# Performance work log

Measured on AMD Instinct MI355X. Metric: run time of the kernel, lower is better.

Reference implementation:

```python
import jax, jax.numpy as jnp
import numpy as np
import math

L = 3        # n_layers
H = 8        # n_heads
D = 128      # embed_dim
KD = D // H  # key_dim = val_dim = 16
FF = 512     # feed_forward_hidden
B, N = 200, 100
BN = B * N
E = 320000
EPS = 1e-5   # BatchNorm1d eps


def setup_inputs() -> dict:
    key = jax.random.key(0)
    ks = jax.random.split(key, 12)

    def u(k, shape, last):  # torch uniform(-1/sqrt(last), 1/sqrt(last)) init
        s = 1.0 / math.sqrt(last)
        return jax.random.uniform(k, shape, jnp.float32, -s, s)

    x = jax.random.normal(ks[0], (B, N, D), jnp.float32)
    edge_index = jax.random.randint(ks[1], (2, E), 0, BN, jnp.int32)
    return {
        "x": x,
        "edge_index": edge_index,
        "Wq": u(ks[2], (L, H, D, KD), KD),
        "Wk": u(ks[3], (L, H, D, KD), KD),
        "Wv": u(ks[4], (L, H, D, KD), KD),
        "Wout": u(ks[5], (L, H, KD, D), D),
        "bn1_w": jnp.ones((L, D), jnp.float32),
        "bn1_b": jnp.zeros((L, D), jnp.float32),
        "W1": u(ks[6], (L, D, FF), D),
        "b1": u(ks[7], (L, FF), D),
        "W2": u(ks[8], (L, FF, D), FF),
        "b2": u(ks[9], (L, D), FF),
        "bn2_w": jnp.ones((L, D), jnp.float32),
        "bn2_b": jnp.zeros((L, D), jnp.float32),
    }


def _batch_norm(h, w, b):
    # BatchNorm1d over flattened (B*N, D), training-mode batch stats (biased var)
    flat = h.reshape(-1, h.shape[-1])
    mu = flat.mean(axis=0)
    var = flat.var(axis=0)
    y = (flat - mu) / jnp.sqrt(var + EPS) * w + b
    return y.reshape(h.shape)


def _gat_conv(h, src, dst, Wq, Wk, Wv, Wout):
    Bb, Nn, Dd = h.shape
    bn = Bb * Nn
    flat = h.reshape(bn, Dd)
    Hh, _, Kk = Wq.shape
    # faithful to torch: matmul gives [H, BN, K], then raw .view(BN, H, K)
    Q = jnp.einsum('nd,hdk->hnk', flat, Wq).reshape(bn, Hh, Kk)
    Kt = jnp.einsum('nd,hdk->hnk', flat, Wk).reshape(bn, Hh, Kk)
    V = jnp.einsum('nd,hdk->hnk', flat, Wv).reshape(bn, Hh, Kk)
    norm = 1.0 / math.sqrt(Kk)
    # message: Q_j (source) . K_i (target) per edge, per head -> [E, H]
    attn = norm * jnp.sum(Q[src] * Kt[dst], axis=-1)
    # segment softmax over edges grouped by target node (max detached, as in PyG)
    m = jax.lax.stop_gradient(jax.ops.segment_max(attn, dst, num_segments=bn))
    ex = jnp.exp(attn - m[dst])
    s = jax.ops.segment_sum(ex, dst, num_segments=bn)
    a = ex / (s[dst] + 1e-16)
    # weighted V_i scatter-added into target nodes -> [BN, H, K]
    aggr = jax.ops.segment_sum(V[dst] * a[:, :, None], dst, num_segments=bn)
    out = aggr.reshape(bn, Hh * Kk) @ Wout.reshape(Hh * Kk, -1)
    return out.reshape(Bb, Nn, -1)


def reference(x, edge_index, Wq, Wk, Wv, Wout, bn1_w, bn1_b, W1, b1, W2, b2, bn2_w, bn2_b):
    src, dst = edge_index[0], edge_index[1]
    h = x
    for l in range(L):
        h = h + _gat_conv(h, src, dst, Wq[l], Wk[l], Wv[l], Wout[l])
        h = _batch_norm(h, bn1_w[l], bn1_b[l])
        ff = jnp.maximum(h @ W1[l] + b1[l], 0.0) @ W2[l] + b2[l]
        h = h + ff
        h = _batch_norm(h, bn2_w[l], bn2_b[l])
    return h
```

## Files before the change

### kernel.cpp

```cpp
#include <hip/hip_runtime.h>
#include <hip/hip_bf16.h>

#define BN_ 20000
#define D_ 128
#define FF_ 512
#define E_ 320000
#define NBLK 313
#define LSTR 136
#define TSTR 72
#define B2STR 72

typedef __attribute__((ext_vector_type(8))) short bf16x8;
typedef __attribute__((ext_vector_type(4))) float f32x4;

__device__ __forceinline__ unsigned short f2b(float f) {
    unsigned int u = __float_as_uint(f);
    u = (u + 0x7FFFu + ((u >> 16) & 1u)) >> 16;
    return (unsigned short)u;
}

__device__ __forceinline__ void make_ss(const float* __restrict__ acc,
                                        const float* __restrict__ w,
                                        const float* __restrict__ b,
                                        float* __restrict__ ss_sh, int tid) {
    if (tid < 128) {
        if (acc) {
            float s = acc[tid], q = acc[128 + tid];
            float mu  = s * (1.f / 20000.f);
            float var = fmaxf(q * (1.f / 20000.f) - mu * mu, 0.f);
            float rstd  = rsqrtf(var + 1e-5f);
            float scale = w[tid] * rstd;
            ss_sh[tid]       = scale;
            ss_sh[128 + tid] = b[tid] - mu * scale;
        } else {
            ss_sh[tid]       = 1.f;
            ss_sh[128 + tid] = 0.f;
        }
    }
}

__global__ __launch_bounds__(256) void k_prep(const float* __restrict__ Wv,
                                              const float* __restrict__ Wout,
                                              const float* __restrict__ W1,
                                              const float* __restrict__ W2,
                                              unsigned short* __restrict__ WcT,
                                              unsigned short* __restrict__ WoT,
                                              unsigned short* __restrict__ W1T,
                                              unsigned short* __restrict__ W2T,
                                              float* __restrict__ flag,
                                              float* __restrict__ acc6) {
    int idx = blockIdx.x * 256 + threadIdx.x;
    if (idx < 49152) {
        int l = idx / 16384, r = idx % 16384;
        int n = r >> 7, k = r & 127;
        int h = n >> 4, kk = n & 15;
        WcT[idx] = f2b(Wv[((l * 8 + h) * 128 + k) * 16 + kk]);
        return;
    }
    idx -= 49152;
    if (idx < 49152) {
        int l = idx / 16384, r = idx % 16384;
        int n = r >> 7, k = r & 127;
        WoT[idx] = f2b(Wout[l * 16384 + k * 128 + n]);
        return;
    }
    idx -= 49152;
    if (idx < 196608) {
        int l = idx / 65536, r = idx % 65536;
        int n = r >> 7, k = r & 127;
        W1T[idx] = f2b(W1[l * 65536 + k * 512 + n]);
        return;
    }
    idx -= 196608;
    if (idx < 196608) {
        int l = idx / 65536, r = idx % 65536;
        int n = r / 512, k = r % 512;
        W2T[idx] = f2b(W2[l * 65536 + k * 128 + n]);
        return;
    }
    idx -= 196608;
    if (idx < 20000) { flag[idx] = 0.f; return; }
    idx -= 20000;
    if (idx < 1536) acc6[idx] = 0.f;
}

__global__ __launch_bounds__(256) void k_flag(const int* __restrict__ dst,
                                              float* __restrict__ flag) {
    int e = blockIdx.x * 256 + threadIdx.x;
    if (e < E_) flag[dst[e]] = 1.0f;
}


__global__ __launch_bounds__(256) void k_vs(const float* __restrict__ H,
                                            const float* __restrict__ accP,
                                            const float* __restrict__ bnw,
                                            const float* __restrict__ bnb,
                                            const unsigned short* __restrict__ Bt,
                                            unsigned short* __restrict__ Vs) {
    __shared__ unsigned short As[64 * LSTR];
    __shared__ unsigned short Bs[64 * LSTR];
    __shared__ float ss_sh[256];
    const int tid = threadIdx.x;
    const int row0 = blockIdx.x * 64, col0 = blockIdx.y * 64;
    make_ss(accP, bnw, bnb, ss_sh, tid);
    __syncthreads();
#pragma unroll
    for (int it = 0; it < 4; ++it) {
        int idx = tid + it * 256;
        int m = idx >> 4, k0 = (idx & 15) << 3;
        int gr = row0 + m;
        float v[8];
        if (gr < BN_) {
            f32x4 v0 = *(const f32x4*)(H + gr * D_ + k0);
            f32x4 v1 = *(const f32x4*)(H + gr * D_ + k0 + 4);
            v[0] = v0.x; v[1] = v0.y; v[2] = v0.z; v[3] = v0.w;
            v[4] = v1.x; v[5] = v1.y; v[6] = v1.z; v[7] = v1.w;
        } else {
#pragma unroll
            for (int j = 0; j < 8; ++j) v[j] = 0.f;
        }
        unsigned int p[4];
#pragma unroll
        for (int j = 0; j < 4; ++j) {
            unsigned short lo = f2b(v[2 * j] * ss_sh[k0 + 2 * j] + ss_sh[128 + k0 + 2 * j]);
            unsigned short hi = f2b(v[2 * j + 1] * ss_sh[k0 + 2 * j + 1] + ss_sh[128 + k0 + 2 * j + 1]);
            p[j] = (unsigned int)lo | ((unsigned int)hi << 16);
        }
        *(uint4*)&As[m * LSTR + k0] = make_uint4(p[0], p[1], p[2], p[3]);
    }
#pragma unroll
    for (int it = 0; it < 4; ++it) {
        int idx = tid + it * 256;
        int n = idx >> 4, k0 = (idx & 15) << 3;
        *(uint4*)&Bs[n * LSTR + k0] = *(const uint4*)(Bt + (col0 + n) * D_ + k0);
    }
    __syncthreads();
    const int lane = tid & 63, wave = tid >> 6;
    const int l16 = lane & 15, quad = lane >> 4;
    const int wm = (wave >> 1) * 32, wn = (wave & 1) * 32;
    f32x4 acc[2][2] = {};
#pragma unroll
    for (int kb = 0; kb < 128; kb += 32) {
        bf16x8 a0 = *(bf16x8*)&As[(wm + l16) * LSTR + kb + quad * 8];
        bf16x8 a1 = *(bf16x8*)&As[(wm + 16 + l16) * LSTR + kb + quad * 8];
        bf16x8 b0 = *(bf16x8*)&Bs[(wn + l16) * LSTR + kb + quad * 8];
        bf16x8 b1 = *(bf16x8*)&Bs[(wn + 16 + l16) * LSTR + kb + quad * 8];
        acc[0][0] = __builtin_amdgcn_mfma_f32_16x16x32_bf16(a0, b0, acc[0][0], 0, 0, 0);
        acc[0][1] = __builtin_amdgcn_mfma_f32_16x16x32_bf16(a0, b1, acc[0][1], 0, 0, 0);
        acc[1][0] = __builtin_amdgcn_mfma_f32_16x16x32_bf16(a1, b0, acc[1][0], 0, 0, 0);
        acc[1][1] = __builtin_amdgcn_mfma_f32_16x16x32_bf16(a1, b1, acc[1][1], 0, 0, 0);
    }
#pragma unroll
    for (int i = 0; i < 2; ++i)
#pragma unroll
        for (int j = 0; j < 2; ++j) {
            int gc = col0 + wn + j * 16 + l16;
            int h = gc >> 4, kk = gc & 15;
#pragma unroll
            for (int r = 0; r < 4; ++r) {
                int gr = row0 + wm + i * 16 + quad * 4 + r;
                if (gr < BN_) Vs[h * (BN_ * 16) + gr * 16 + kk] = f2b(acc[i][j][r]);
            }
        }
}

__global__ __launch_bounds__(256) void k_out(const unsigned short* __restrict__ Vs,
                                             const unsigned short* __restrict__ Bt,
                                             const float* __restrict__ H,
                                             const float* __restrict__ accP,
                                             const float* __restrict__ bnw,
                                             const float* __restrict__ bnb,
                                             const float* __restrict__ flag,
                                             float* __restrict__ H1,
                                             float* __restrict__ accO) {
    __shared__ unsigned short As[64 * LSTR];
    __shared__ unsigned short Bs[64 * LSTR];
    __shared__ float ss_sh[256];
    const int tid = threadIdx.x;
    const int row0 = blockIdx.x * 64, col0 = blockIdx.y * 64;
    make_ss(accP, bnw, bnb, ss_sh, tid);
#pragma unroll
    for (int it = 0; it < 4; ++it) {
        int idx = tid + it * 256;
        int m = idx >> 4, k0 = (idx & 15) << 3;
        int gr = row0 + m;
        uint4 w = make_uint4(0u, 0u, 0u, 0u);
        if (gr < BN_) w = *(const uint4*)(Vs + gr * D_ + k0);
        *(uint4*)&As[m * LSTR + k0] = w;
    }
#pragma unroll
    for (int it = 0; it < 4; ++it) {
        int idx = tid + it * 256;
        int n = idx >> 4, k0 = (idx & 15) << 3;
        *(uint4*)&Bs[n * LSTR + k0] = *(const uint4*)(Bt + (col0 + n) * D_ + k0);
    }
    __syncthreads();
    const int lane = tid & 63, wave = tid >> 6;
    const int l16 = lane & 15, quad = lane >> 4;
    const int wm = (wave >> 1) * 32, wn = (wave & 1) * 32;
    f32x4 acc[2][2] = {};
#pragma unroll
    for (int kb = 0; kb < 128; kb += 32) {
        bf16x8 a0 = *(bf16x8*)&As[(wm + l16) * LSTR + kb + quad * 8];
        bf16x8 a1 = *(bf16x8*)&As[(wm + 16 + l16) * LSTR + kb + quad * 8];
        bf16x8 b0 = *(bf16x8*)&Bs[(wn + l16) * LSTR + kb + quad * 8];
        bf16x8 b1 = *(bf16x8*)&Bs[(wn + 16 + l16) * LSTR + kb + quad * 8];
        acc[0][0] = __builtin_amdgcn_mfma_f32_16x16x32_bf16(a0, b0, acc[0][0], 0, 0, 0);
        acc[0][1] = __builtin_amdgcn_mfma_f32_16x16x32_bf16(a0, b1, acc[0][1], 0, 0, 0);
        acc[1][0] = __builtin_amdgcn_mfma_f32_16x16x32_bf16(a1, b0, acc[1][0], 0, 0, 0);
        acc[1][1] = __builtin_amdgcn_mfma_f32_16x16x32_bf16(a1, b1, acc[1][1], 0, 0, 0);
    }
    __syncthreads();
    float* Sred = (float*)As;
    float* Qred = (float*)Bs;
    const int slot = (wave >> 1) * 4 + quad;
#pragma unroll
    for (int j = 0; j < 2; ++j) {
        int gc = col0 + wn + j * 16 + l16;
        float sc = ss_sh[gc & 127];
        float sh = ss_sh[128 + (gc & 127)];
        float cs = 0.f, cq = 0.f;
#pragma unroll
        for (int i = 0; i < 2; ++i)
#pragma unroll
            for (int r = 0; r < 4; ++r) {
                int gr = row0 + wm + i * 16 + quad * 4 + r;
                if (gr < BN_) {
                    float z = H[gr * D_ + gc] * sc + sh;
                    float o = z + flag[gr] * acc[i][j][r];
                    H1[gr * D_ + gc] = o;
                    cs += o; cq += o * o;
                }
            }
        Sred[(wn + j * 16 + l16) * 8 + slot] = cs;
        Qred[(wn + j * 16 + l16) * 8 + slot] = cq;
    }
    __syncthreads();
    if (tid < 64) {
        float s = 0.f, q = 0.f;
#pragma unroll
        for (int t = 0; t < 8; ++t) { s += Sred[tid * 8 + t]; q += Qred[tid * 8 + t]; }
        atomicAdd(&accO[col0 + tid], s);
        atomicAdd(&accO[128 + col0 + tid], q);
    }
}

__global__ __launch_bounds__(256) void k_ff(const float* __restrict__ H1,
                                            const float* __restrict__ accP,
                                            const float* __restrict__ bnw,
                                            const float* __restrict__ bnb,
                                            const unsigned short* __restrict__ W1t,
                                            const float* __restrict__ b1l,
                                            const unsigned short* __restrict__ W2t,
                                            const float* __restrict__ b2l,
                                            float* __restrict__ H2,
                                            float* __restrict__ accO) {
    __shared__ unsigned short As[64 * LSTR];
    __shared__ unsigned short Bs[64 * LSTR];
    __shared__ unsigned short B2[128 * B2STR];
    __shared__ unsigned short Tch[64 * TSTR];
    __shared__ float ss_sh[256];
    const int tid = threadIdx.x;
    const int row0 = blockIdx.x * 64;
    make_ss(accP, bnw, bnb, ss_sh, tid);
    __syncthreads();
#pragma unroll
    for (int it = 0; it < 4; ++it) {
        int idx = tid + it * 256;
        int m = idx >> 4, k0 = (idx & 15) << 3;
        int gr = row0 + m;
        float v[8];
        if (gr < BN_) {
            f32x4 v0 = *(const f32x4*)(H1 + gr * D_ + k0);
            f32x4 v1 = *(const f32x4*)(H1 + gr * D_ + k0 + 4);
            v[0] = v0.x; v[1] = v0.y; v[2] = v0.z; v[3] = v0.w;
            v[4] = v1.x; v[5] = v1.y; v[6] = v1.z; v[7] = v1.w;
        } else {
#pragma unroll
            for (int j = 0; j < 8; ++j) v[j] = 0.f;
        }
        unsigned int p[4];
#pragma unroll
        for (int j = 0; j < 4; ++j) {
            unsigned short lo = f2b(v[2 * j] * ss_sh[k0 + 2 * j] + ss_sh[128 + k0 + 2 * j]);
            unsigned short hi = f2b(v[2 * j + 1] * ss_sh[k0 + 2 * j + 1] + ss_sh[128 + k0 + 2 * j + 1]);
            p[j] = (unsigned int)lo | ((unsigned int)hi << 16);
        }
        *(uint4*)&As[m * LSTR + k0] = make_uint4(p[0], p[1], p[2], p[3]);
    }
    const int lane = tid & 63, wave = tid >> 6;
    const int l16 = lane & 15, quad = lane >> 4;
    const int wm = (wave >> 1) * 32;
    const int wn = (wave & 1) * 32;
    const int wn2 = (wave & 1) * 64;
    f32x4 acc2[2][4] = {};
    for (int c = 0; c < 8; ++c) {
        const int cb = c * 64;
        __syncthreads();
#pragma unroll
        for (int it = 0; it < 4; ++it) {
            int idx = tid + it * 256;
            int n = idx >> 4, k0 = (idx & 15) << 3;
            *(uint4*)&Bs[n * LSTR + k0] = *(const uint4*)(W1t + (cb + n) * D_ + k0);
        }
#pragma unroll
        for (int it = 0; it < 4; ++it) {
            int idx = tid + it * 256;
            int n = idx >> 3, k0 = (idx & 7) << 3;
            *(uint4*)&B2[n * B2STR + k0] = *(const uint4*)(W2t + n * FF_ + cb + k0);
        }
        __syncthreads();
        f32x4 acc1[2][2] = {};
#pragma unroll
        for (int kb = 0; kb < 128; kb += 32) {
            bf16x8 a0 = *(bf16x8*)&As[(wm + l16) * LSTR + kb + quad * 8];
            bf16x8 a1 = *(bf16x8*)&As[(wm + 16 + l16) * LSTR + kb + quad * 8];
            bf16x8 b0 = *(bf16x8*)&Bs[(wn + l16) * LSTR + kb + quad * 8];
            bf16x8 b1 = *(bf16x8*)&Bs[(wn + 16 + l16) * LSTR + kb + quad * 8];
            acc1[0][0] = __builtin_amdgcn_mfma_f32_16x16x32_bf16(a0, b0, acc1[0][0], 0, 0, 0);
            acc1[0][1] = __builtin_amdgcn_mfma_f32_16x16x32_bf16(a0, b1, acc1[0][1], 0, 0, 0);
            acc1[1][0] = __builtin_amdgcn_mfma_f32_16x16x32_bf16(a1, b0, acc1[1][0], 0, 0, 0);
            acc1[1][1] = __builtin_amdgcn_mfma_f32_16x16x32_bf16(a1, b1, acc1[1][1], 0, 0, 0);
        }
#pragma unroll
        for (int j = 0; j < 2; ++j) {
            int lc = wn + j * 16 + l16;
            float bb = b1l[cb + lc];
#pragma unroll
            for (int i = 0; i < 2; ++i)
#pragma unroll
                for (int r = 0; r < 4; ++r)
                    Tch[(wm + i * 16 + quad * 4 + r) * TSTR + lc] =
                        f2b(fmaxf(acc1[i][j][r] + bb, 0.f));
        }
        __syncthreads();
#pragma unroll
        for (int kb = 0; kb < 64; kb += 32) {
            bf16x8 a0 = *(bf16x8*)&Tch[(wm + l16) * TSTR + kb + quad * 8];
            bf16x8 a1 = *(bf16x8*)&Tch[(wm + 16 + l16) * TSTR + kb + quad * 8];
#pragma unroll
            for (int j2 = 0; j2 < 4; ++j2) {
                bf16x8 b = *(bf16x8*)&B2[(wn2 + j2 * 16 + l16) * B2STR + kb + quad * 8];
                acc2[0][j2] = __builtin_amdgcn_mfma_f32_16x16x32_bf16(a0, b, acc2[0][j2], 0, 0, 0);
                acc2[1][j2] = __builtin_amdgcn_mfma_f32_16x16x32_bf16(a1, b, acc2[1][j2], 0, 0, 0);
            }
        }
    }
    __syncthreads();
    float* Sred = (float*)As;
    float* Qred = (float*)Bs;
    const int slot = (wave >> 1) * 4 + quad;
#pragma unroll
    for (int j2 = 0; j2 < 4; ++j2) {
        int gc = wn2 + j2 * 16 + l16;
        float sc = ss_sh[gc], sh = ss_sh[128 + gc], bb = b2l[gc];
        float cs = 0.f, cq = 0.f;
#pragma unroll
        for (int i = 0; i < 2; ++i)
#pragma unroll
            for (int r = 0; r < 4; ++r) {
                int gr = row0 + wm + i * 16 + quad * 4 + r;
                if (gr < BN_) {
                    float o = H1[gr * D_ + gc] * sc + sh + acc2[i][j2][r] + bb;
                    H2[gr * D_ + gc] = o;
                    cs += o; cq += o * o;
                }
            }
        Sred[gc * 8 + slot] = cs;
        Qred[gc * 8 + slot] = cq;
    }
    __syncthreads();
    if (tid < 128) {
        float s = 0.f, q = 0.f;
#pragma unroll
        for (int t = 0; t < 8; ++t) { s += Sred[tid * 8 + t]; q += Qred[tid * 8 + t]; }
        atomicAdd(&accO[tid], s);
        atomicAdd(&accO[128 + tid], q);
    }
}

__global__ __launch_bounds__(256) void k_apply(const float4* __restrict__ H2,
                                               const float* __restrict__ accP,
                                               const float* __restrict__ bnw,
                                               const float* __restrict__ bnb,
                                               float4* __restrict__ out) {
    __shared__ float ss_sh[256];
    make_ss(accP, bnw, bnb, ss_sh, threadIdx.x);
    __syncthreads();
    int i = blockIdx.x * 256 + threadIdx.x;
    if (i >= BN_ * D_ / 4) return;
    int c = (i & 31) << 2;
    float4 v = H2[i];
    v.x = v.x * ss_sh[c + 0] + ss_sh[128 + c + 0];
    v.y = v.y * ss_sh[c + 1] + ss_sh[128 + c + 1];
    v.z = v.z * ss_sh[c + 2] + ss_sh[128 + c + 2];
    v.w = v.w * ss_sh[c + 3] + ss_sh[128 + c + 3];
    out[i] = v;
}


extern "C" void kernel_launch(void* const* d_in, const int* in_sizes, int n_in,
                              void* d_out, int out_size, void* d_ws, size_t ws_size,
                              hipStream_t stream) {
    (void)in_sizes; (void)n_in; (void)out_size; (void)ws_size;
    const float* x    = (const float*)d_in[0];
    const int*   edge = (const int*)d_in[1];
    const float* Wv   = (const float*)d_in[4];
    const float* Wout = (const float*)d_in[5];
    const float* bn1w = (const float*)d_in[6];
    const float* bn1b = (const float*)d_in[7];
    const float* W1   = (const float*)d_in[8];
    const float* b1   = (const float*)d_in[9];
    const float* W2   = (const float*)d_in[10];
    const float* b2   = (const float*)d_in[11];
    const float* bn2w = (const float*)d_in[12];
    const float* bn2b = (const float*)d_in[13];

    float* ws   = (float*)d_ws;
    float* bufA = ws;
    float* bufB = ws + 2560000;
    float* flag = ws + 5120000;
    float* acc6 = ws + 5140000;
    unsigned short* Vs  = (unsigned short*)(ws + 5141536);
    unsigned short* WcT = (unsigned short*)(ws + 6421536);
    unsigned short* WoT = (unsigned short*)(ws + 6446112);
    unsigned short* W1T = (unsigned short*)(ws + 6470688);
    unsigned short* W2T = (unsigned short*)(ws + 6568992);

    k_prep<<<2005, 256, 0, stream>>>(Wv, Wout, W1, W2, WcT, WoT, W1T, W2T,
                                     flag, acc6);
    k_flag<<<1250, 256, 0, stream>>>(edge + E_, flag);

    for (int l = 0; l < 3; ++l) {
        const float* Hc   = (l == 0) ? x : bufA;
        const float* accP = (l == 0) ? nullptr : acc6 + (2 * l - 1) * 256;
        float* acc1p = acc6 + (2 * l) * 256;
        float* acc2p = acc6 + (2 * l + 1) * 256;
        const float* bw  = bn2w + (l ? (l - 1) * 128 : 0);
        const float* bbv = bn2b + (l ? (l - 1) * 128 : 0);
        k_vs<<<dim3(NBLK, 2), 256, 0, stream>>>(Hc, accP, bw, bbv,
                                                WcT + l * 16384, Vs);
        k_out<<<dim3(NBLK, 2), 256, 0, stream>>>(Vs, WoT + l * 16384, Hc, accP,
                                                 bw, bbv, flag, bufB, acc1p);
        k_ff<<<NBLK, 256, 0, stream>>>(bufB, acc1p, bn1w + l * 128, bn1b + l * 128,
                                       W1T + l * 65536, b1 + l * 512,
                                       W2T + l * 65536, b2 + l * 128, bufA, acc2p);
    }
    k_apply<<<2500, 256, 0, stream>>>((const float4*)bufA, acc6 + 5 * 256,
                                      bn2w + 256, bn2b + 256, (float4*)d_out);
}
```

Measured before the change: 251.4 us.

## Fuse all layers into one persistent kernel with software grid barriers

Replaces the chain of per-layer launches (prep, flag, vs, out, ff, apply) with a single persistent kernel of 313 blocks that uses an atomic-counter grid barrier between dependent stages. Weight conversion, flag setting, the V/out/FF GEMMs and the final BN apply are all done inside it, with each block owning a 64-row tile. This removes launch gaps and inter-kernel drains. In exchange it relies on all 313 blocks being co-resident, otherwise the barrier deadlocks, and it adds barrier spin cost. The merged kernel's combined LDS footprint may also reduce occupancy.

Result: slower. 950.8 us (+278.2%).

```diff
diff --git a/kernel.cpp b/kernel.cpp
--- a/kernel.cpp
+++ b/kernel.cpp
@@ -5,7 +5,7 @@
 #define D_ 128
 #define FF_ 512
 #define E_ 320000
-#define NBLK 313
+#define NB_ 313
 #define LSTR 136
 #define TSTR 72
 #define B2STR 72
@@ -39,363 +39,373 @@
     }
 }
 
-__global__ __launch_bounds__(256) void k_prep(const float* __restrict__ Wv,
-                                              const float* __restrict__ Wout,
-                                              const float* __restrict__ W1,
-                                              const float* __restrict__ W2,
-                                              unsigned short* __restrict__ WcT,
-                                              unsigned short* __restrict__ WoT,
-                                              unsigned short* __restrict__ W1T,
-                                              unsigned short* __restrict__ W2T,
-                                              float* __restrict__ flag,
-                                              float* __restrict__ acc6) {
-    int idx = blockIdx.x * 256 + threadIdx.x;
-    if (idx < 49152) {
+__device__ __forceinline__ void gbar(int* __restrict__ bar) {
+    __builtin_amdgcn_fence(__ATOMIC_RELEASE, "agent");
+    __syncthreads();
+    if (threadIdx.x == 0) {
+        int* cnt = bar;
+        int* gen = bar + 1;
+        int g = __hip_atomic_load(gen, __ATOMIC_RELAXED, __HIP_MEMORY_SCOPE_AGENT);
+        int prev = __hip_atomic_fetch_add(cnt, 1, __ATOMIC_ACQ_REL, __HIP_MEMORY_SCOPE_AGENT);
+        if (prev == NB_ - 1) {
+            __hip_atomic_store(cnt, 0, __ATOMIC_RELAXED, __HIP_MEMORY_SCOPE_AGENT);
+            __hip_atomic_fetch_add(gen, 1, __ATOMIC_ACQ_REL, __HIP_MEMORY_SCOPE_AGENT);
+        } else {
+            while (__hip_atomic_load(gen, __ATOMIC_RELAXED, __HIP_MEMORY_SCOPE_AGENT) == g)
+                __builtin_amdgcn_s_sleep(2);
+        }
+    }
+    __syncthreads();
+    __builtin_amdgcn_fence(__ATOMIC_ACQUIRE, "agent");
+}
+
+__global__ __launch_bounds__(256) void k_init(float* __restrict__ flag,
+                                              float* __restrict__ acc6,
+                                              int* __restrict__ bar) {
+    int i = blockIdx.x * 256 + threadIdx.x;
+    if (i < BN_) flag[i] = 0.f;
+    if (i < 1536) acc6[i] = 0.f;
+    if (i < 2) bar[i] = 0;
+}
+
+__global__ __launch_bounds__(256, 2) void k_main(
+    const float* __restrict__ x, const int* __restrict__ dst,
+    const float* __restrict__ Wv, const float* __restrict__ Wout,
+    const float* __restrict__ bn1w, const float* __restrict__ bn1b,
+    const float* __restrict__ W1, const float* __restrict__ b1,
+    const float* __restrict__ W2, const float* __restrict__ b2,
+    const float* __restrict__ bn2w, const float* __restrict__ bn2b,
+    float* __restrict__ bufA, float* __restrict__ bufB,
+    float* __restrict__ flag, float* __restrict__ acc6,
+    unsigned short* __restrict__ Vs,
+    unsigned short* __restrict__ WcT, unsigned short* __restrict__ WoT,
+    unsigned short* __restrict__ W1T, unsigned short* __restrict__ W2T,
+    int* __restrict__ bar, float* __restrict__ out) {
+    __shared__ unsigned short As[64 * LSTR];
+    __shared__ unsigned short Bs[64 * LSTR];
+    __shared__ unsigned short B2m[128 * B2STR];
+    __shared__ unsigned short Tch[64 * TSTR];
+    __shared__ float ss_sh[256];
+
+    const int tid = threadIdx.x;
+    const int row0 = blockIdx.x * 64;
+    const int gid = blockIdx.x * 256 + tid;
+    const int gstride = NB_ * 256;
+
+    for (int idx = gid; idx < 49152; idx += gstride) {
         int l = idx / 16384, r = idx % 16384;
         int n = r >> 7, k = r & 127;
         int h = n >> 4, kk = n & 15;
         WcT[idx] = f2b(Wv[((l * 8 + h) * 128 + k) * 16 + kk]);
-        return;
-    }
-    idx -= 49152;
-    if (idx < 49152) {
+    }
+    for (int idx = gid; idx < 49152; idx += gstride) {
         int l = idx / 16384, r = idx % 16384;
         int n = r >> 7, k = r & 127;
         WoT[idx] = f2b(Wout[l * 16384 + k * 128 + n]);
-        return;
-    }
-    idx -= 49152;
-    if (idx < 196608) {
+    }
+    for (int idx = gid; idx < 196608; idx += gstride) {
         int l = idx / 65536, r = idx % 65536;
         int n = r >> 7, k = r & 127;
         W1T[idx] = f2b(W1[l * 65536 + k * 512 + n]);
-        return;
-    }
-    idx -= 196608;
-    if (idx < 196608) {
+    }
+    for (int idx = gid; idx < 196608; idx += gstride) {
         int l = idx / 65536, r = idx % 65536;
         int n = r / 512, k = r % 512;
         W2T[idx] = f2b(W2[l * 65536 + k * 128 + n]);
-        return;
-    }
-    idx -= 196608;
-    if (idx < 20000) { flag[idx] = 0.f; return; }
-    idx -= 20000;
-    if (idx < 1536) acc6[idx] = 0.f;
-}
-
-__global__ __launch_bounds__(256) void k_flag(const int* __restrict__ dst,
-                                              float* __restrict__ flag) {
-    int e = blockIdx.x * 256 + threadIdx.x;
-    if (e < E_) flag[dst[e]] = 1.0f;
-}
-
-
-__global__ __launch_bounds__(256) void k_vs(const float* __restrict__ H,
-                                            const float* __restrict__ accP,
-                                            const float* __restrict__ bnw,
-                                            const float* __restrict__ bnb,
-                                            const unsigned short* __restrict__ Bt,
-                                            unsigned short* __restrict__ Vs) {
-    __shared__ unsigned short As[64 * LSTR];
-    __shared__ unsigned short Bs[64 * LSTR];
-    __shared__ float ss_sh[256];
-    const int tid = threadIdx.x;
-    const int row0 = blockIdx.x * 64, col0 = blockIdx.y * 64;
-    make_ss(accP, bnw, bnb, ss_sh, tid);
-    __syncthreads();
-#pragma unroll
-    for (int it = 0; it < 4; ++it) {
-        int idx = tid + it * 256;
-        int m = idx >> 4, k0 = (idx & 15) << 3;
-        int gr = row0 + m;
-        float v[8];
-        if (gr < BN_) {
-            f32x4 v0 = *(const f32x4*)(H + gr * D_ + k0);
-            f32x4 v1 = *(const f32x4*)(H + gr * D_ + k0 + 4);
-            v[0] = v0.x; v[1] = v0.y; v[2] = v0.z; v[3] = v0.w;
-            v[4] = v1.x; v[5] = v1.y; v[6] = v1.z; v[7] = v1.w;
-        } else {
-#pragma unroll
-            for (int j = 0; j < 8; ++j) v[j] = 0.f;
-        }
-        unsigned int p[4];
-#pragma unroll
-        for (int j = 0; j < 4; ++j) {
-            unsigned short lo = f2b(v[2 * j] * ss_sh[k0 + 2 * j] + ss_sh[128 + k0 + 2 * j]);
-            unsigned short hi = f2b(v[2 * j + 1] * ss_sh[k0 + 2 * j + 1] + ss_sh[128 + k0 + 2 * j + 1]);
-            p[j] = (unsigned int)lo | ((unsigned int)hi << 16);
-        }
-        *(uint4*)&As[m * LSTR + k0] = make_uint4(p[0], p[1], p[2], p[3]);
-    }
-#pragma unroll
-    for (int it = 0; it < 4; ++it) {
-        int idx = tid + it * 256;
-        int n = idx >> 4, k0 = (idx & 15) << 3;
-        *(uint4*)&Bs[n * LSTR + k0] = *(const uint4*)(Bt + (col0 + n) * D_ + k0);
-    }
-    __syncthreads();
-    const int lane = tid & 63, wave = tid >> 6;
-    const int l16 = lane & 15, quad = lane >> 4;
-    const int wm = (wave >> 1) * 32, wn = (wave & 1) * 32;
-    f32x4 acc[2][2] = {};
-#pragma unroll
-    for (int kb = 0; kb < 128; kb += 32) {
-        bf16x8 a0 = *(bf16x8*)&As[(wm + l16) * LSTR + kb + quad * 8];
-        bf16x8 a1 = *(bf16x8*)&As[(wm + 16 + l16) * LSTR + kb + quad * 8];
-        bf16x8 b0 = *(bf16x8*)&Bs[(wn + l16) * LSTR + kb + quad * 8];
-        bf16x8 b1 = *(bf16x8*)&Bs[(wn + 16 + l16) * LSTR + kb + quad * 8];
-        acc[0][0] = __builtin_amdgcn_mfma_f32_16x16x32_bf16(a0, b0, acc[0][0], 0, 0, 0);
-        acc[0][1] = __builtin_amdgcn_mfma_f32_16x16x32_bf16(a0, b1, acc[0][1], 0, 0, 0);
-        acc[1][0] = __builtin_amdgcn_mfma_f32_16x16x32_bf16(a1, b0, acc[1][0], 0, 0, 0);
-        acc[1][1] = __builtin_amdgcn_mfma_f32_16x16x32_bf16(a1, b1, acc[1][1], 0, 0, 0);
-    }
-#pragma unroll
-    for (int i = 0; i < 2; ++i)
-#pragma unroll
-        for (int j = 0; j < 2; ++j) {
-            int gc = col0 + wn + j * 16 + l16;
-            int h = gc >> 4, kk = gc & 15;
-#pragma unroll
-            for (int r = 0; r < 4; ++r) {
-                int gr = row0 + wm + i * 16 + quad * 4 + r;
-                if (gr < BN_) Vs[h * (BN_ * 16) + gr * 16 + kk] = f2b(acc[i][j][r]);
-            }
-        }
-}
-
-__global__ __launch_bounds__(256) void k_out(const unsigned short* __restrict__ Vs,
-                                             const unsigned short* __restrict__ Bt,
-                                             const float* __restrict__ H,
-                                             const float* __restrict__ accP,
-                                             const float* __restrict__ bnw,
-                                             const float* __restrict__ bnb,
-                                             const float* __restrict__ flag,
-                                             float* __restrict__ H1,
-                                             float* __restrict__ accO) {
-    __shared__ unsigned short As[64 * LSTR];
-    __shared__ unsigned short Bs[64 * LSTR];
-    __shared__ float ss_sh[256];
-    const int tid = threadIdx.x;
-    const int row0 = blockIdx.x * 64, col0 = blockIdx.y * 64;
-    make_ss(accP, bnw, bnb, ss_sh, tid);
-#pragma unroll
-    for (int it = 0; it < 4; ++it) {
-        int idx = tid + it * 256;
-        int m = idx >> 4, k0 = (idx & 15) << 3;
-        int gr = row0 + m;
-        uint4 w = make_uint4(0u, 0u, 0u, 0u);
-        if (gr < BN_) w = *(const uint4*)(Vs + gr * D_ + k0);
-        *(uint4*)&As[m * LSTR + k0] = w;
-    }
-#pragma unroll
-    for (int it = 0; it < 4; ++it) {
-        int idx = tid + it * 256;
-        int n = idx >> 4, k0 = (idx & 15) << 3;
-        *(uint4*)&Bs[n * LSTR + k0] = *(const uint4*)(Bt + (col0 + n) * D_ + k0);
-    }
-    __syncthreads();
-    const int lane = tid & 63, wave = tid >> 6;
-    const int l16 = lane & 15, quad = lane >> 4;
-    const int wm = (wave >> 1) * 32, wn = (wave & 1) * 32;
-    f32x4 acc[2][2] = {};
-#pragma unroll
-    for (int kb = 0; kb < 128; kb += 32) {
-        bf16x8 a0 = *(bf16x8*)&As[(wm + l16) * LSTR + kb + quad * 8];
-        bf16x8 a1 = *(bf16x8*)&As[(wm + 16 + l16) * LSTR + kb + quad * 8];
-        bf16x8 b0 = *(bf16x8*)&Bs[(wn + l16) * LSTR + kb + quad * 8];
-        bf16x8 b1 = *(bf16x8*)&Bs[(wn + 16 + l16) * LSTR + kb + quad * 8];
-        acc[0][0] = __builtin_amdgcn_mfma_f32_16x16x32_bf16(a0, b0, acc[0][0], 0, 0, 0);
-        acc[0][1] = __builtin_amdgcn_mfma_f32_16x16x32_bf16(a0, b1, acc[0][1], 0, 0, 0);
-        acc[1][0] = __builtin_amdgcn_mfma_f32_16x16x32_bf16(a1, b0, acc[1][0], 0, 0, 0);
-        acc[1][1] = __builtin_amdgcn_mfma_f32_16x16x32_bf16(a1, b1, acc[1][1], 0, 0, 0);
-    }
-    __syncthreads();
-    float* Sred = (float*)As;
-    float* Qred = (float*)Bs;
-    const int slot = (wave >> 1) * 4 + quad;
-#pragma unroll
-    for (int j = 0; j < 2; ++j) {
-        int gc = col0 + wn + j * 16 + l16;
-        float sc = ss_sh[gc & 127];
-        float sh = ss_sh[128 + (gc & 127)];
-        float cs = 0.f, cq = 0.f;
-#pragma unroll
-        for (int i = 0; i < 2; ++i)
-#pragma unroll
-            for (int r = 0; r < 4; ++r) {
-                int gr = row0 + wm + i * 16 + quad * 4 + r;
-                if (gr < BN_) {
-                    float z = H[gr * D_ + gc] * sc + sh;
-                    float o = z + flag[gr] * acc[i][j][r];
-                    H1[gr * D_ + gc] = o;
-                    cs += o; cq += o * o;
-                }
-            }
-        Sred[(wn + j * 16 + l16) * 8 + slot] = cs;
-        Qred[(wn + j * 16 + l16) * 8 + slot] = cq;
-    }
-    __syncthreads();
-    if (tid < 64) {
-        float s = 0.f, q = 0.f;
-#pragma unroll
-        for (int t = 0; t < 8; ++t) { s += Sred[tid * 8 + t]; q += Qred[tid * 8 + t]; }
-        atomicAdd(&accO[col0 + tid], s);
-        atomicAdd(&accO[128 + col0 + tid], q);
-    }
-}
-
-__global__ __launch_bounds__(256) void k_ff(const float* __restrict__ H1,
-                                            const float* __restrict__ accP,
-                                            const float* __restrict__ bnw,
-                                            const float* __restrict__ bnb,
-                                            const unsigned short* __restrict__ W1t,
-                                            const float* __restrict__ b1l,
-                                            const unsigned short* __restrict__ W2t,
-                                            const float* __restrict__ b2l,
-                                            float* __restrict__ H2,
-                                            float* __restrict__ accO) {
-    __shared__ unsigned short As[64 * LSTR];
-    __shared__ unsigned short Bs[64 * LSTR];
-    __shared__ unsigned short B2[128 * B2STR];
-    __shared__ unsigned short Tch[64 * TSTR];
-    __shared__ float ss_sh[256];
-    const int tid = threadIdx.x;
-    const int row0 = blockIdx.x * 64;
-    make_ss(accP, bnw, bnb, ss_sh, tid);
-    __syncthreads();
-#pragma unroll
-    for (int it = 0; it < 4; ++it) {
-        int idx = tid + it * 256;
-        int m = idx >> 4, k0 = (idx & 15) << 3;
-        int gr = row0 + m;
-        float v[8];
-        if (gr < BN_) {
-            f32x4 v0 = *(const f32x4*)(H1 + gr * D_ + k0);
-            f32x4 v1 = *(const f32x4*)(H1 + gr * D_ + k0 + 4);
-            v[0] = v0.x; v[1] = v0.y; v[2] = v0.z; v[3] = v0.w;
-            v[4] = v1.x; v[5] = v1.y; v[6] = v1.z; v[7] = v1.w;
-        } else {
-#pragma unroll
-            for (int j = 0; j < 8; ++j) v[j] = 0.f;
-        }
-        unsigned int p[4];
-#pragma unroll
-        for (int j = 0; j < 4; ++j) {
-            unsigned short lo = f2b(v[2 * j] * ss_sh[k0 + 2 * j] + ss_sh[128 + k0 + 2 * j]);
-            unsigned short hi = f2b(v[2 * j + 1] * ss_sh[k0 + 2 * j + 1] + ss_sh[128 + k0 + 2 * j + 1]);
-            p[j] = (unsigned int)lo | ((unsigned int)hi << 16);
-        }
-        *(uint4*)&As[m * LSTR + k0] = make_uint4(p[0], p[1], p[2], p[3]);
-    }
+    }
+    for (int e = gid; e < E_; e += gstride) flag[dst[e]] = 1.0f;
+
+    gbar(bar);
+
     const int lane = tid & 63, wave = tid >> 6;
     const int l16 = lane & 15, quad = lane >> 4;
     const int wm = (wave >> 1) * 32;
     const int wn = (wave & 1) * 32;
     const int wn2 = (wave & 1) * 64;
-    f32x4 acc2[2][4] = {};
-    for (int c = 0; c < 8; ++c) {
-        const int cb = c * 64;
+
+    for (int l = 0; l < 3; ++l) {
+        const float* Hc   = (l == 0) ? x : bufA;
+        const float* accP = (l == 0) ? nullptr : acc6 + (2 * l - 1) * 256;
+        const float* bw   = bn2w + (l ? (l - 1) * 128 : 0);
+        const float* bbv  = bn2b + (l ? (l - 1) * 128 : 0);
+        float* acc1p = acc6 + (2 * l) * 256;
+        float* acc2p = acc6 + (2 * l + 1) * 256;
+        const unsigned short* Wc_l = WcT + l * 16384;
+        const unsigned short* Wo_l = WoT + l * 16384;
+        const unsigned short* W1_l = W1T + l * 65536;
+        const unsigned short* W2_l = W2T + l * 65536;
+        const float* b1_l = b1 + l * 512;
+        const float* b2_l = b2 + l * 128;
+
+        make_ss(accP, bw, bbv, ss_sh, tid);
         __syncthreads();
 #pragma unroll
         for (int it = 0; it < 4; ++it) {
             int idx = tid + it * 256;
-            int n = idx >> 4, k0 = (idx & 15) << 3;
-            *(uint4*)&Bs[n * LSTR + k0] = *(const uint4*)(W1t + (cb + n) * D_ + k0);
-        }
+            int m = idx >> 4, k0 = (idx & 15) << 3;
+            int gr = row0 + m;
+            float v[8];
+            if (gr < BN_) {
+                f32x4 v0 = *(const f32x4*)(Hc + gr * D_ + k0);
+                f32x4 v1 = *(const f32x4*)(Hc + gr * D_ + k0 + 4);
+                v[0] = v0.x; v[1] = v0.y; v[2] = v0.z; v[3] = v0.w;
+                v[4] = v1.x; v[5] = v1.y; v[6] = v1.z; v[7] = v1.w;
+            } else {
+#pragma unroll
+                for (int j = 0; j < 8; ++j) v[j] = 0.f;
+            }
+            unsigned int p[4];
+#pragma unroll
+            for (int j = 0; j < 4; ++j) {
+                unsigned short lo = f2b(v[2 * j] * ss_sh[k0 + 2 * j] + ss_sh[128 + k0 + 2 * j]);
+                unsigned short hi = f2b(v[2 * j + 1] * ss_sh[k0 + 2 * j + 1] + ss_sh[128 + k0 + 2 * j + 1]);
+                p[j] = (unsigned int)lo | ((unsigned int)hi << 16);
+            }
+            *(uint4*)&As[m * LSTR + k0] = make_uint4(p[0], p[1], p[2], p[3]);
+        }
+#pragma unroll
+        for (int half = 0; half < 2; ++half) {
+            const int col0 = half * 64;
+            if (half) __syncthreads();
+#pragma unroll
+            for (int it = 0; it < 4; ++it) {
+                int idx = tid + it * 256;
+                int n = idx >> 4, k0 = (idx & 15) << 3;
+                *(uint4*)&Bs[n * LSTR + k0] = *(const uint4*)(Wc_l + (col0 + n) * D_ + k0);
+            }
+            __syncthreads();
+            f32x4 acc[2][2] = {};
+#pragma unroll
+            for (int kb = 0; kb < 128; kb += 32) {
+                bf16x8 a0 = *(bf16x8*)&As[(wm + l16) * LSTR + kb + quad * 8];
+                bf16x8 a1 = *(bf16x8*)&As[(wm + 16 + l16) * LSTR + kb + quad * 8];
+                bf16x8 b0 = *(bf16x8*)&Bs[(wn + l16) * LSTR + kb + quad * 8];
+                bf16x8 b1 = *(bf16x8*)&Bs[(wn + 16 + l16) * LSTR + kb + quad * 8];
+                acc[0][0] = __builtin_amdgcn_mfma_f32_16x16x32_bf16(a0, b0, acc[0][0], 0, 0, 0);
+                acc[0][1] = __builtin_amdgcn_mfma_f32_16x16x32_bf16(a0, b1, acc[0][1], 0, 0, 0);
+                acc[1][0] = __builtin_amdgcn_mfma_f32_16x16x32_bf16(a1, b0, acc[1][0], 0, 0, 0);
+                acc[1][1] = __builtin_amdgcn_mfma_f32_16x16x32_bf16(a1, b1, acc[1][1], 0, 0, 0);
+            }
+#pragma unroll
+            for (int i = 0; i < 2; ++i)
+#pragma unroll
+                for (int j = 0; j < 2; ++j) {
+                    int gc = col0 + wn + j * 16 + l16;
+                    int h = gc >> 4, kk = gc & 15;
+#pragma unroll
+                    for (int r = 0; r < 4; ++r) {
+                        int gr = row0 + wm + i * 16 + quad * 4 + r;
+                        if (gr < BN_) Vs[h * (BN_ * 16) + gr * 16 + kk] = f2b(acc[i][j][r]);
+                    }
+                }
+        }
+
+        gbar(bar);
+
 #pragma unroll
         for (int it = 0; it < 4; ++it) {
             int idx = tid + it * 256;
-            int n = idx >> 3, k0 = (idx & 7) << 3;
-            *(uint4*)&B2[n * B2STR + k0] = *(const uint4*)(W2t + n * FF_ + cb + k0);
+            int m = idx >> 4, k0 = (idx & 15) << 3;
+            int gr = row0 + m;
+            uint4 w = make_uint4(0u, 0u, 0u, 0u);
+            if (gr < BN_) w = *(const uint4*)(Vs + gr * D_ + k0);
+            *(uint4*)&As[m * LSTR + k0] = w;
+        }
+        f32x4 acc3[2][2][2] = {};
+#pragma unroll
+        for (int half = 0; half < 2; ++half) {
+            const int col0 = half * 64;
+            if (half) __syncthreads();
+#pragma unroll
+            for (int it = 0; it < 4; ++it) {
+                int idx = tid + it * 256;
+                int n = idx >> 4, k0 = (idx & 15) << 3;
+                *(uint4*)&Bs[n * LSTR + k0] = *(const uint4*)(Wo_l + (col0 + n) * D_ + k0);
+            }
+            __syncthreads();
+#pragma unroll
+            for (int kb = 0; kb < 128; kb += 32) {
+                bf16x8 a0 = *(bf16x8*)&As[(wm + l16) * LSTR + kb + quad * 8];
+                bf16x8 a1 = *(bf16x8*)&As[(wm + 16 + l16) * LSTR + kb + quad * 8];
+                bf16x8 b0 = *(bf16x8*)&Bs[(wn + l16) * LSTR + kb + quad * 8];
+                bf16x8 b1 = *(bf16x8*)&Bs[(wn + 16 + l16) * LSTR + kb + quad * 8];
+                acc3[half][0][0] = __builtin_amdgcn_mfma_f32_16x16x32_bf16(a0, b0, acc3[half][0][0], 0, 0, 0);
+                acc3[half][0][1] = __builtin_amdgcn_mfma_f32_16x16x32_bf16(a0, b1, acc3[half][0][1], 0, 0, 0);
+                acc3[half][1][0] = __builtin_amdgcn_mfma_f32_16x16x32_bf16(a1, b0, acc3[half][1][0], 0, 0, 0);
+                acc3[half][1][1] = __builtin_amdgcn_mfma_f32_16x16x32_bf16(a1, b1, acc3[half][1][1], 0, 0, 0);
+            }
         }
         __syncthreads();
-        f32x4 acc1[2][2] = {};
-#pragma unroll
-        for (int kb = 0; kb < 128; kb += 32) {
-            bf16x8 a0 = *(bf16x8*)&As[(wm + l16) * LSTR + kb + quad * 8];
-            bf16x8 a1 = *(bf16x8*)&As[(wm + 16 + l16) * LSTR + kb + quad * 8];
-            bf16x8 b0 = *(bf16x8*)&Bs[(wn + l16) * LSTR + kb + quad * 8];
-            bf16x8 b1 = *(bf16x8*)&Bs[(wn + 16 + l16) * LSTR + kb + quad * 8];
-            acc1[0][0] = __builtin_amdgcn_mfma_f32_16x16x32_bf16(a0, b0, acc1[0][0], 0, 0, 0);
-            acc1[0][1] = __builtin_amdgcn_mfma_f32_16x16x32_bf16(a0, b1, acc1[0][1], 0, 0, 0);
-            acc1[1][0] = __builtin_amdgcn_mfma_f32_16x16x32_bf16(a1, b0, acc1[1][0], 0, 0, 0);
-            acc1[1][1] = __builtin_amdgcn_mfma_f32_16x16x32_bf16(a1, b1, acc1[1][1], 0, 0, 0);
-        }
-#pragma unroll
-        for (int j = 0; j < 2; ++j) {
-            int lc = wn + j * 16 + l16;
-            float bb = b1l[cb + lc];
-#pragma unroll
-            for (int i = 0; i < 2; ++i)
-#pragma unroll
-                for (int r = 0; r < 4; ++r)
-                    Tch[(wm + i * 16 + quad * 4 + r) * TSTR + lc] =
-                        f2b(fmaxf(acc1[i][j][r] + bb, 0.f));
-        }
+        {
+            float* Sred = (float*)As;
+            float* Qred = (float*)Bs;
+            const int slot = (wave >> 1) * 4 + quad;
+#pragma unroll
+            for (int half = 0; half < 2; ++half)
+#pragma unroll
+                for (int j = 0; j < 2; ++j) {
+                    int gc = half * 64 + wn + j * 16 + l16;
+                    float sc = ss_sh[gc], sh = ss_sh[128 + gc];
+                    float cs = 0.f, cq = 0.f;
+#pragma unroll
+                    for (int i = 0; i < 2; ++i)
+#pragma unroll
+                        for (int r = 0; r < 4; ++r) {
+                            int gr = row0 + wm + i * 16 + quad * 4 + r;
+                            if (gr < BN_) {
+                                float z = Hc[gr * D_ + gc] * sc + sh;
+                                float o = z + flag[gr] * acc3[half][i][j][r];
+                                bufB[gr * D_ + gc] = o;
+                                cs += o; cq += o * o;
+                            }
+                        }
+                    Sred[gc * 8 + slot] = cs;
+                    Qred[gc * 8 + slot] = cq;
+                }
+            __syncthreads();
+            if (tid < 128) {
+                float s = 0.f, q = 0.f;
+#pragma unroll
+                for (int t = 0; t < 8; ++t) { s += Sred[tid * 8 + t]; q += Qred[tid * 8 + t]; }
+                atomicAdd(&acc1p[tid], s);
+                atomicAdd(&acc1p[128 + tid], q);
+            }
+        }
+
+        gbar(bar);
+
+        make_ss(acc1p, bn1w + l * 128, bn1b + l * 128, ss_sh, tid);
         __syncthreads();
 #pragma unroll
-        for (int kb = 0; kb < 64; kb += 32) {
-            bf16x8 a0 = *(bf16x8*)&Tch[(wm + l16) * TSTR + kb + quad * 8];
-            bf16x8 a1 = *(bf16x8*)&Tch[(wm + 16 + l16) * TSTR + kb + quad * 8];
+        for (int it = 0; it < 4; ++it) {
+            int idx = tid + it * 256;
+            int m = idx >> 4, k0 = (idx & 15) << 3;
+            int gr = row0 + m;
+            float v[8];
+            if (gr < BN_) {
+                f32x4 v0 = *(const f32x4*)(bufB + gr * D_ + k0);
+                f32x4 v1 = *(const f32x4*)(bufB + gr * D_ + k0 + 4);
+                v[0] = v0.x; v[1] = v0.y; v[2] = v0.z; v[3] = v0.w;
+                v[4] = v1.x; v[5] = v1.y; v[6] = v1.z; v[7] = v1.w;
+            } else {
+#pragma unroll
+                for (int j = 0; j < 8; ++j) v[j] = 0.f;
+            }
+            unsigned int p[4];
+#pragma unroll
+            for (int j = 0; j < 4; ++j) {
+                unsigned short lo = f2b(v[2 * j] * ss_sh[k0 + 2 * j] + ss_sh[128 + k0 + 2 * j]);
+                unsigned short hi = f2b(v[2 * j + 1] * ss_sh[k0 + 2 * j + 1] + ss_sh[128 + k0 + 2 * j + 1]);
+                p[j] = (unsigned int)lo | ((unsigned int)hi << 16);
+            }
+            *(uint4*)&As[m * LSTR + k0] = make_uint4(p[0], p[1], p[2], p[3]);
+        }
+        f32x4 acc2[2][4] = {};
+        for (int c = 0; c < 8; ++c) {
+            const int cb = c * 64;
+            __syncthreads();
+#pragma unroll
+            for (int it = 0; it < 4; ++it) {
+                int idx = tid + it * 256;
+                int n = idx >> 4, k0 = (idx & 15) << 3;
+                *(uint4*)&Bs[n * LSTR + k0] = *(const uint4*)(W1_l + (cb + n) * D_ + k0);
+            }
+#pragma unroll
+            for (int it = 0; it < 4; ++it) {
+                int idx = tid + it * 256;
+                int n = idx >> 3, k0 = (idx & 7) << 3;
+                *(uint4*)&B2m[n * B2STR + k0] = *(const uint4*)(W2_l + n * FF_ + cb + k0);
+            }
+            __syncthreads();
+            f32x4 acc1[2][2] = {};
+#pragma unroll
+            for (int kb = 0; kb < 128; kb += 32) {
+                bf16x8 a0 = *(bf16x8*)&As[(wm + l16) * LSTR + kb + quad * 8];
+                bf16x8 a1 = *(bf16x8*)&As[(wm + 16 + l16) * LSTR + kb + quad * 8];
+                bf16x8 b0 = *(bf16x8*)&Bs[(wn + l16) * LSTR + kb + quad * 8];
+                bf16x8 b1 = *(bf16x8*)&Bs[(wn + 16 + l16) * LSTR + kb + quad * 8];
+                acc1[0][0] = __builtin_amdgcn_mfma_f32_16x16x32_bf16(a0, b0, acc1[0][0], 0, 0, 0);
+                acc1[0][1] = __builtin_amdgcn_mfma_f32_16x16x32_bf16(a0, b1, acc1[0][1], 0, 0, 0);
+                acc1[1][0] = __builtin_amdgcn_mfma_f32_16x16x32_bf16(a1, b0, acc1[1][0], 0, 0, 0);
+                acc1[1][1] = __builtin_amdgcn_mfma_f32_16x16x32_bf16(a1, b1, acc1[1][1], 0, 0, 0);
+            }
+#pragma unroll
+            for (int j = 0; j < 2; ++j) {
+                int lc = wn + j * 16 + l16;
+                float bb = b1_l[cb + lc];
+#pragma unroll
+                for (int i = 0; i < 2; ++i)
+#pragma unroll
+                    for (int r = 0; r < 4; ++r)
+                        Tch[(wm + i * 16 + quad * 4 + r) * TSTR + lc] =
+                            f2b(fmaxf(acc1[i][j][r] + bb, 0.f));
+            }
+            __syncthreads();
+#pragma unroll
+            for (int kb = 0; kb < 64; kb += 32) {
+                bf16x8 a0 = *(bf16x8*)&Tch[(wm + l16) * TSTR + kb + quad * 8];
+                bf16x8 a1 = *(bf16x8*)&Tch[(wm + 16 + l16) * TSTR + kb + quad * 8];
+#pragma unroll
+                for (int j2 = 0; j2 < 4; ++j2) {
+                    bf16x8 b = *(bf16x8*)&B2m[(wn2 + j2 * 16 + l16) * B2STR + kb + quad * 8];
+                    acc2[0][j2] = __builtin_amdgcn_mfma_f32_16x16x32_bf16(a0, b, acc2[0][j2], 0, 0, 0);
+                    acc2[1][j2] = __builtin_amdgcn_mfma_f32_16x16x32_bf16(a1, b, acc2[1][j2], 0, 0, 0);
+                }
+            }
+        }
+        __syncthreads();
+        {
+            float* Sred = (float*)As;
+            float* Qred = (float*)Bs;
+            const int slot = (wave >> 1) * 4 + quad;
 #pragma unroll
             for (int j2 = 0; j2 < 4; ++j2) {
-                bf16x8 b = *(bf16x8*)&B2[(wn2 + j2 * 16 + l16) * B2STR + kb + quad * 8];
-                acc2[0][j2] = __builtin_amdgcn_mfma_f32_16x16x32_bf16(a0, b, acc2[0][j2], 0, 0, 0);
-                acc2[1][j2] = __builtin_amdgcn_mfma_f32_16x16x32_bf16(a1, b, acc2[1][j2], 0, 0, 0);
-            }
-        }
-    }
+                int gc = wn2 + j2 * 16 + l16;
+                float sc = ss_sh[gc], sh = ss_sh[128 + gc], bb = b2_l[gc];
+                float cs = 0.f, cq = 0.f;
+#pragma unroll
+                for (int i = 0; i < 2; ++i)
+#pragma unroll
+                    for (int r = 0; r < 4; ++r) {
+                        int gr = row0 + wm + i * 16 + quad * 4 + r;
+                        if (gr < BN_) {
+                            float o = bufB[gr * D_ + gc] * sc + sh + acc2[i][j2][r] + bb;
+                            bufA[gr * D_ + gc] = o;
+                            cs += o; cq += o * o;
+                        }
+                    }
+                Sred[gc * 8 + slot] = cs;
+                Qred[gc * 8 + slot] = cq;
+            }
+            __syncthreads();
+            if (tid < 128) {
+                float s = 0.f, q = 0.f;
+#pragma unroll
+                for (int t = 0; t < 8; ++t) { s += Sred[tid * 8 + t]; q += Qred[tid * 8 + t]; }
+                atomicAdd(&acc2p[tid], s);
+                atomicAdd(&acc2p[128 + tid], q);
+            }
+        }
+
+        gbar(bar);
+    }
+
+    make_ss(acc6 + 5 * 256, bn2w + 256, bn2b + 256, ss_sh, tid);
     __syncthreads();
-    float* Sred = (float*)As;
-    float* Qred = (float*)Bs;
-    const int slot = (wave >> 1) * 4 + quad;
-#pragma unroll
-    for (int j2 = 0; j2 < 4; ++j2) {
-        int gc = wn2 + j2 * 16 + l16;
-        float sc = ss_sh[gc], sh = ss_sh[128 + gc], bb = b2l[gc];
-        float cs = 0.f, cq = 0.f;
-#pragma unroll
-        for (int i = 0; i < 2; ++i)
-#pragma unroll
-            for (int r = 0; r < 4; ++r) {
-                int gr = row0 + wm + i * 16 + quad * 4 + r;
-                if (gr < BN_) {
-                    float o = H1[gr * D_ + gc] * sc + sh + acc2[i][j2][r] + bb;
-                    H2[gr * D_ + gc] = o;
-                    cs += o; cq += o * o;
-                }
-            }
-        Sred[gc * 8 + slot] = cs;
-        Qred[gc * 8 + slot] = cq;
-    }
-    __syncthreads();
-    if (tid < 128) {
-        float s = 0.f, q = 0.f;
-#pragma unroll
-        for (int t = 0; t < 8; ++t) { s += Sred[tid * 8 + t]; q += Qred[tid * 8 + t]; }
-        atomicAdd(&accO[tid], s);
-        atomicAdd(&accO[128 + tid], q);
-    }
-}
-
-__global__ __launch_bounds__(256) void k_apply(const float4* __restrict__ H2,
-                                               const float* __restrict__ accP,
-                                               const float* __restrict__ bnw,
-                                               const float* __restrict__ bnb,
-                                               float4* __restrict__ out) {
-    __shared__ float ss_sh[256];
-    make_ss(accP, bnw, bnb, ss_sh, threadIdx.x);
-    __syncthreads();
-    int i = blockIdx.x * 256 + threadIdx.x;
-    if (i >= BN_ * D_ / 4) return;
-    int c = (i & 31) << 2;
-    float4 v = H2[i];
-    v.x = v.x * ss_sh[c + 0] + ss_sh[128 + c + 0];
-    v.y = v.y * ss_sh[c + 1] + ss_sh[128 + c + 1];
-    v.z = v.z * ss_sh[c + 2] + ss_sh[128 + c + 2];
-    v.w = v.w * ss_sh[c + 3] + ss_sh[128 + c + 3];
-    out[i] = v;
+#pragma unroll
+    for (int it = 0; it < 8; ++it) {
+        int idx = tid + it * 256;
+        int m = idx >> 5, c4 = (idx & 31) << 2;
+        int gr = row0 + m;
+        if (gr < BN_) {
+            f32x4 v = *(const f32x4*)(bufA + gr * D_ + c4);
+            v.x = v.x * ss_sh[c4 + 0] + ss_sh[128 + c4 + 0];
+            v.y = v.y * ss_sh[c4 + 1] + ss_sh[128 + c4 + 1];
+            v.z = v.z * ss_sh[c4 + 2] + ss_sh[128 + c4 + 2];
+            v.w = v.w * ss_sh[c4 + 3] + ss_sh[128 + c4 + 3];
+            *(f32x4*)(out + gr * D_ + c4) = v;
+        }
+    }
 }
 
 
@@ -421,31 +431,15 @@
     float* bufB = ws + 2560000;
     float* flag = ws + 5120000;
     float* acc6 = ws + 5140000;
-    unsigned short* Vs  = (unsigned short*)(ws + 5141536);
-    unsigned short* WcT = (unsigned short*)(ws + 6421536);
-    unsigned short* WoT = (unsigned short*)(ws + 6446112);
-    unsigned short* W1T = (unsigned short*)(ws + 6470688);
-    unsigned short* W2T = (unsigned short*)(ws + 6568992);
-
-    k_prep<<<2005, 256, 0, stream>>>(Wv, Wout, W1, W2, WcT, WoT, W1T, W2T,
-                                     flag, acc6);
-    k_flag<<<1250, 256, 0, stream>>>(edge + E_, flag);
-
-    for (int l = 0; l < 3; ++l) {
-        const float* Hc   = (l == 0) ? x : bufA;
-        const float* accP = (l == 0) ? nullptr : acc6 + (2 * l - 1) * 256;
-        float* acc1p = acc6 + (2 * l) * 256;
-        float* acc2p = acc6 + (2 * l + 1) * 256;
-        const float* bw  = bn2w + (l ? (l - 1) * 128 : 0);
-        const float* bbv = bn2b + (l ? (l - 1) * 128 : 0);
-        k_vs<<<dim3(NBLK, 2), 256, 0, stream>>>(Hc, accP, bw, bbv,
-                                                WcT + l * 16384, Vs);
-        k_out<<<dim3(NBLK, 2), 256, 0, stream>>>(Vs, WoT + l * 16384, Hc, accP,
-                                                 bw, bbv, flag, bufB, acc1p);
-        k_ff<<<NBLK, 256, 0, stream>>>(bufB, acc1p, bn1w + l * 128, bn1b + l * 128,
-                                       W1T + l * 65536, b1 + l * 512,
-                                       W2T + l * 65536, b2 + l * 128, bufA, acc2p);
-    }
-    k_apply<<<2500, 256, 0, stream>>>((const float4*)bufA, acc6 + 5 * 256,
-                                      bn2w + 256, bn2b + 256, (float4*)d_out);
-}
+    int*   bar  = (int*)(ws + 5141536);
+    unsigned short* Vs  = (unsigned short*)(ws + 5141540);
+    unsigned short* WcT = (unsigned short*)(ws + 6421540);
+    unsigned short* WoT = (unsigned short*)(ws + 6446116);
+    unsigned short* W1T = (unsigned short*)(ws + 6470692);
+    unsigned short* W2T = (unsigned short*)(ws + 6568996);
+
+    k_init<<<79, 256, 0, stream>>>(flag, acc6, bar);
+    k_main<<<NB_, 256, 0, stream>>>(x, edge + E_, Wv, Wout, bn1w, bn1b, W1, b1,
+                                    W2, b2, bn2w, bn2b, bufA, bufB, flag, acc6,
+                                    Vs, WcT, WoT, W1T, W2T, bar, (float*)d_out);
+}
```
